# Kernel optimization log

Hardware: AMD Instinct MI355X
Metric: run time of the kernel (lower is better)

The kernel has to match this reference:

```python
import jax, jax.numpy as jnp
import numpy as np
from jax import lax

B_, H_, W_, C_ = 2, 64, 64, 96
DI, N_, R_, K_ = 192, 16, 6, 4  # d_inner=expand*C, d_state, dt_rank=ceil(96/16), 4 scan dirs


def _ln(x, g, b, eps):
    m = jnp.mean(x, axis=-1, keepdims=True)
    v = jnp.var(x, axis=-1, keepdims=True)
    return (x - m) / jnp.sqrt(v + eps) * g + b


def _conv1x1(x, w, b=None):
    y = jnp.einsum('bihw,oi->bohw', x, w)
    return y if b is None else y + b[None, :, None, None]


def _dwconv(x, w):
    return lax.conv_general_dilated(x, w, (1, 1), 'SAME',
                                    feature_group_count=x.shape[1],
                                    dimension_numbers=('NCHW', 'OIHW', 'NCHW'))


def _ss2d(x, in_proj_w, conv2d_w, conv2d_b, x_proj_w, dt_proj_w, dt_proj_b,
          A_logs, Ds, out_norm_g, out_norm_b, out_proj_w):
    B, H, W, C = x.shape
    L = H * W
    xz = jnp.einsum('bhwc,dc->bhwd', x, in_proj_w)          # [B,H,W,2*DI]
    xx, z = jnp.split(xz, 2, axis=-1)
    xc = jnp.transpose(xx, (0, 3, 1, 2))                    # [B,DI,H,W]
    xc = jax.nn.silu(_dwconv(xc, conv2d_w) + conv2d_b[None, :, None, None])
    # 4 scan directions: row-major, col-major, and their reverses
    x_hwwh = jnp.stack([xc.reshape(B, DI, L),
                        jnp.transpose(xc, (0, 1, 3, 2)).reshape(B, DI, L)], axis=1)
    xs = jnp.concatenate([x_hwwh, jnp.flip(x_hwwh, axis=-1)], axis=1)  # [B,K,DI,L]
    x_dbl = jnp.einsum('bkdl,kcd->bkcl', xs, x_proj_w)
    dts, Bs, Cs = jnp.split(x_dbl, [R_, R_ + N_], axis=2)   # [B,K,R,L],[B,K,N,L],[B,K,N,L]
    dt = jnp.einsum('bkrl,kdr->bkdl', dts, dt_proj_w) + dt_proj_b[None, :, :, None]
    dt = jax.nn.softplus(dt)
    A = -jnp.exp(A_logs).reshape(K_, DI, N_)

    def step(h, inp):
        u_t, dt_t, B_t, C_t = inp                            # [B,K,DI],[B,K,DI],[B,K,N],[B,K,N]
        dA = jnp.exp(dt_t[..., None] * A)                    # [B,K,DI,N]
        h = h * dA + (dt_t * u_t)[..., None] * B_t[:, :, None, :]
        y = jnp.einsum('bkdn,bkn->bkd', h, C_t)
        return h, y

    inps = (jnp.moveaxis(xs, -1, 0), jnp.moveaxis(dt, -1, 0),
            jnp.moveaxis(Bs, -1, 0), jnp.moveaxis(Cs, -1, 0))
    h0 = jnp.zeros((B, K_, DI, N_), xs.dtype)
    _, ys = lax.scan(step, h0, inps)                         # [L,B,K,DI]
    out_y = jnp.moveaxis(ys, 0, -1) + xs * Ds.reshape(K_, DI)[None, :, :, None]
    inv = jnp.flip(out_y[:, 2:4], axis=-1)
    y1 = out_y[:, 0]
    y2 = inv[:, 0]
    y3 = jnp.transpose(out_y[:, 1].reshape(B, DI, W, H), (0, 1, 3, 2)).reshape(B, DI, L)
    y4 = jnp.transpose(inv[:, 1].reshape(B, DI, W, H), (0, 1, 3, 2)).reshape(B, DI, L)
    y = jnp.transpose(y1 + y2 + y3 + y4, (0, 2, 1)).reshape(B, H, W, DI)
    y = _ln(y, out_norm_g, out_norm_b, 1e-5)
    y = y * jax.nn.silu(z)
    return jnp.einsum('bhwd,cd->bhwc', y, out_proj_w)


def _fftm(x, f1_w, f1_b, fm_w, fm_b, f2_w, f2_b):
    x = jax.nn.silu(_conv1x1(x, f1_w, f1_b))                 # [B,C/2,H,W]
    f = jnp.fft.rfftn(x, axes=(-2, -1), norm='ortho')        # [B,C/2,H,W//2+1] complex
    B, Ch, Hh, Wf = f.shape
    fr = jnp.stack([f.real, f.imag], axis=2).reshape(B, 2 * Ch, Hh, Wf)
    fr = jax.nn.silu(_conv1x1(fr, fm_w, fm_b))
    fr = fr.reshape(B, Ch, 2, Hh, Wf)
    fc = lax.complex(fr[:, :, 0], fr[:, :, 1])
    out = jnp.fft.irfftn(fc, s=x.shape[-2:], axes=(-2, -1), norm='ortho')
    return _conv1x1(out, f2_w, f2_b)


def _mgcb(x, in_w, dw3_w, dw5_w, out_w, ca_w1, ca_b1, ca_w2, ca_b2):
    Hd = 2 * x.shape[1]                                      # hidden_features = 2*dim
    p = _conv1x1(x, in_w)                                    # [B,2*Hd,H,W]
    s1 = 3 * Hd // 2
    x1, x2 = p[:, :s1], p[:, s1:]
    d1 = _dwconv(x1, dw3_w)
    x1_1, x1_2 = d1[:, :Hd], d1[:, Hd:]
    x2 = _dwconv(x2, dw5_w)
    y = jax.nn.gelu(x1_1, approximate=False) * jnp.concatenate([x1_2, x2], axis=1)
    y = _conv1x1(y, out_w)
    a = jnp.mean(y, axis=(2, 3))                             # channel attention (squeeze 30)
    a = jax.nn.relu(a @ ca_w1.T + ca_b1)
    a = jax.nn.sigmoid(a @ ca_w2.T + ca_b2)
    return y * a[:, :, None, None]


def _forward(input, ln1_g, ln1_b, skip_scale, skip_scale2, ln2_g, ln2_b,
             in_proj_w, conv2d_w, conv2d_b, x_proj_w, dt_proj_w, dt_proj_b,
             A_logs, Ds, out_norm_g, out_norm_b, out_proj_w,
             f1_w, f1_b, fm_w, fm_b, f2_w, f2_b,
             mg_in_w, mg_dw3_w, mg_dw5_w, mg_out_w,
             ca_w1, ca_b1, ca_w2, ca_b2, h_size, w_size):
    B, L, C = input.shape
    x4 = input.reshape(B, h_size, w_size, C)
    xn = _ln(x4, ln1_g, ln1_b, 1e-6)
    attn = _ss2d(xn, in_proj_w, conv2d_w, conv2d_b, x_proj_w, dt_proj_w,
                 dt_proj_b, A_logs, Ds, out_norm_g, out_norm_b, out_proj_w)
    fft = _fftm(jnp.transpose(xn, (0, 3, 1, 2)), f1_w, f1_b, fm_w, fm_b, f2_w, f2_b)
    x = x4 * skip_scale + attn + jnp.transpose(fft, (0, 2, 3, 1))
    xn2 = _ln(x, ln2_g, ln2_b, 1e-5)
    conv = _mgcb(jnp.transpose(xn2, (0, 3, 1, 2)), mg_in_w, mg_dw3_w, mg_dw5_w,
                 mg_out_w, ca_w1, ca_b1, ca_w2, ca_b2)
    x = x * skip_scale2 + jnp.transpose(conv, (0, 2, 3, 1))
    return x.reshape(B, L, C)


def setup_inputs() -> dict:
    key = jax.random.key(0)
    ks = iter(jax.random.split(key, 48))
    def rn(shape, s=0.02):
        return jax.random.normal(next(ks), shape, jnp.float32) * s
    d = {}
    d['input'] = jax.random.normal(next(ks), (B_, H_ * W_, C_), jnp.float32)
    d['ln1_g'] = jnp.ones((C_,)); d['ln1_b'] = jnp.zeros((C_,))
    d['skip_scale'] = jnp.ones((C_,)); d['skip_scale2'] = jnp.ones((C_,))
    d['ln2_g'] = jnp.ones((C_,)); d['ln2_b'] = jnp.zeros((C_,))
    d['in_proj_w'] = rn((2 * DI, C_))
    d['conv2d_w'] = rn((DI, 1, 3, 3), 0.1); d['conv2d_b'] = jnp.zeros((DI,))
    d['x_proj_w'] = rn((K_, R_ + 2 * N_, DI))
    d['dt_proj_w'] = rn((K_, DI, R_), 0.1)
    d['dt_proj_b'] = jnp.full((K_, DI), -4.6, jnp.float32) + rn((K_, DI), 0.5)
    d['A_logs'] = jnp.log(jnp.tile(jnp.arange(1, N_ + 1, dtype=jnp.float32), (K_ * DI, 1)))
    d['Ds'] = jnp.ones((K_ * DI,))
    d['out_norm_g'] = jnp.ones((DI,)); d['out_norm_b'] = jnp.zeros((DI,))
    d['out_proj_w'] = rn((C_, DI))
    Ch = C_ // 2
    d['f1_w'] = rn((Ch, C_)); d['f1_b'] = jnp.zeros((Ch,))
    d['fm_w'] = rn((C_, C_)); d['fm_b'] = jnp.zeros((C_,))
    d['f2_w'] = rn((C_, Ch)); d['f2_b'] = jnp.zeros((C_,))
    Hd = 2 * C_
    d['mg_in_w'] = rn((2 * Hd, C_))
    d['mg_dw3_w'] = rn((3 * Hd // 2, 1, 3, 3), 0.1)
    d['mg_dw5_w'] = rn((Hd // 2, 1, 5, 5), 0.1)
    d['mg_out_w'] = rn((C_, Hd))
    Csq = C_ // 30
    d['ca_w1'] = rn((Csq, C_)); d['ca_b1'] = jnp.zeros((Csq,))
    d['ca_w2'] = rn((C_, Csq)); d['ca_b2'] = jnp.zeros((C_,))
    d['h_size'] = H_
    d['w_size'] = W_
    return d


def reference(input, ln1_g, ln1_b, skip_scale, skip_scale2, ln2_g, ln2_b,
              in_proj_w, conv2d_w, conv2d_b, x_proj_w, dt_proj_w, dt_proj_b,
              A_logs, Ds, out_norm_g, out_norm_b, out_proj_w,
              f1_w, f1_b, fm_w, fm_b, f2_w, f2_b,
              mg_in_w, mg_dw3_w, mg_dw5_w, mg_out_w,
              ca_w1, ca_b1, ca_w2, ca_b2, h_size, w_size):
    return _forward(input, ln1_g, ln1_b, skip_scale, skip_scale2, ln2_g, ln2_b,
                    in_proj_w, conv2d_w, conv2d_b, x_proj_w, dt_proj_w, dt_proj_b,
                    A_logs, Ds, out_norm_g, out_norm_b, out_proj_w,
                    f1_w, f1_b, fm_w, fm_b, f2_w, f2_b,
                    mg_in_w, mg_dw3_w, mg_dw5_w, mg_out_w,
                    ca_w1, ca_b1, ca_w2, ca_b2, h_size, w_size)
```

## Files before the change

### kernel.cpp

```cpp
#include <hip/hip_runtime.h>
#include <math.h>

#define DEV __device__ __forceinline__

constexpr int DI = 192, Nn = 16, Rr = 6;
constexpr int Cc = 96;
constexpr int Ll = 4096;
constexpr int NC = 64;

DEV float silu_(float x) { return x / (1.f + __expf(-x)); }
DEV float wsum64(float v) {
  #pragma unroll
  for (int m = 32; m; m >>= 1) v += __shfl_xor(v, m, 64);
  return v;
}
DEV float qadd1(float v) {
  int i = __builtin_amdgcn_mov_dpp(__float_as_int(v), 0xB1, 0xF, 0xF, true);
  return v + __int_as_float(i);
}
DEV float qadd2(float v) {
  int i = __builtin_amdgcn_mov_dpp(__float_as_int(v), 0x4E, 0xF, 0xF, true);
  return v + __int_as_float(i);
}

template<int CIN, int COUT, int CB, int PXB, int IN_MODE, int OUT_MODE, int ACT, int HAS_BIAS, int LN>
__global__ void conv1x1v2_kernel(const float* __restrict__ in, const float4* __restrict__ wt,
                                 const float* __restrict__ bias, float* __restrict__ out,
                                 float* __restrict__ out2, const float* __restrict__ lng,
                                 const float* __restrict__ lnb) {
  constexpr int J4 = CIN / 4, STR = J4 + 1, CCN = CB / 16, PXT = PXB / 16;
  constexpr int NPB = 8192 / PXB;
  __shared__ float4 xv[PXB * STR];
  int t = threadIdx.x;
  int pb = blockIdx.x % NPB;
  int cbase = (blockIdx.x / NPB) * CB;
  int pbase = pb * PXB;
  if (IN_MODE == 0) {
    for (int idx = t; idx < PXB * J4; idx += 256) {
      int px = idx / J4, j4 = idx - px * J4;
      xv[px * STR + j4] = ((const float4*)in)[(size_t)(pbase + px) * J4 + j4];
    }
  } else {
    for (int idx = t; idx < PXB * CIN; idx += 256) {
      int px = idx & (PXB - 1), c = idx / PXB;
      int gp = pbase + px; int b = gp >> 12, p = gp & 4095;
      ((float*)xv)[px * (STR * 4) + c] = in[((size_t)b * CIN + c) * Ll + p];
    }
  }
  __syncthreads();
  if constexpr (LN) {
    constexpr int TPX = 256 / PXB;
    constexpr int CHUNK = CIN / TPX;
    int px = t / TPX, sub = t % TPX;
    float* row = (float*)(xv + px * STR);
    float sm = 0.f, sq = 0.f;
    #pragma unroll
    for (int j2 = 0; j2 < CHUNK; ++j2) {
      float v = row[sub + j2 * TPX];
      sm += v; sq += v * v;
    }
    #pragma unroll
    for (int m = 1; m < TPX; m <<= 1) {
      sm += __shfl_xor(sm, m, 64);
      sq += __shfl_xor(sq, m, 64);
    }
    float mean = sm * (1.f / CIN);
    float rs = rsqrtf(sq * (1.f / CIN) - mean * mean + 1e-6f);
    #pragma unroll
    for (int j2 = 0; j2 < CHUNK; ++j2) {
      int j = sub + j2 * TPX;
      row[j] = (row[j] - mean) * rs * lng[j] + lnb[j];
    }
    __syncthreads();
  }
  int g = t >> 4, ci = t & 15;
  float acc[PXT][CCN];
  #pragma unroll
  for (int cc = 0; cc < CCN; ++cc) {
    float b0 = HAS_BIAS ? bias[cbase + ci + 16 * cc] : 0.f;
    #pragma unroll
    for (int p = 0; p < PXT; ++p) acc[p][cc] = b0;
  }
  #pragma unroll 2
  for (int j4 = 0; j4 < J4; ++j4) {
    float4 xr[PXT];
    #pragma unroll
    for (int p = 0; p < PXT; ++p) xr[p] = xv[(g + 16 * p) * STR + j4];
    #pragma unroll
    for (int cc = 0; cc < CCN; ++cc) {
      float4 w4 = wt[(size_t)j4 * COUT + cbase + ci + 16 * cc];
      #pragma unroll
      for (int p = 0; p < PXT; ++p)
        acc[p][cc] += xr[p].x * w4.x + xr[p].y * w4.y + xr[p].z * w4.z + xr[p].w * w4.w;
    }
  }
  #pragma unroll
  for (int p = 0; p < PXT; ++p) {
    int gp = pbase + g + 16 * p;
    #pragma unroll
    for (int cc = 0; cc < CCN; ++cc) {
      int c = cbase + ci + 16 * cc;
      float v = acc[p][cc];
      if (OUT_MODE == 2) {
        if (c < 192) out[(size_t)gp * 192 + c] = v;
        else out2[(size_t)gp * 192 + (c - 192)] = silu_(v);
      } else {
        if (ACT == 1) v = silu_(v);
        if (OUT_MODE == 0) out[(size_t)gp * COUT + c] = v;
        else { int bb = gp >> 12, p2 = gp & 4095; out[((size_t)bb * COUT + c) * Ll + p2] = v; }
      }
    }
  }
}

__global__ void wprep_all_kernel(const float* __restrict__ xpw, float4* __restrict__ xpwT,
                                 const float* __restrict__ cw, const float* __restrict__ mg3,
                                 const float* __restrict__ mg5, float* __restrict__ WC3T,
                                 float* __restrict__ W3T, float* __restrict__ W5T,
                                 const float* __restrict__ ipw, float4* __restrict__ WIPT,
                                 const float* __restrict__ mgiw, float4* __restrict__ WMGT,
                                 const float* __restrict__ opw, float4* __restrict__ WOPT,
                                 const float* __restrict__ mgow, float4* __restrict__ WMOT,
                                 const float* __restrict__ f1w, float4* __restrict__ WF1T,
                                 const float* __restrict__ f2w, float4* __restrict__ WF2T) {
  int idx = blockIdx.x * 256 + threadIdx.x;
  if (idx < 9216) {
    int k = idx / (48 * 48);
    int r = idx % (48 * 48);
    int j4 = r / 48, c = r % 48;
    float4 v = make_float4(0.f, 0.f, 0.f, 0.f);
    if (c < 38) v = ((const float4*)xpw)[((size_t)k * 38 + c) * 48 + j4];
    xpwT[((size_t)k * 48 + j4) * 48 + c] = v;
  }
  if (idx < 1728) { int c = idx / 9, j = idx % 9; WC3T[j * 192 + c] = cw[idx]; }
  if (idx < 2592) { int c = idx / 9, j = idx % 9; W3T[j * 288 + c] = mg3[idx]; }
  if (idx < 2400) { int c = idx / 25, j = idx % 25; W5T[j * 96 + c] = mg5[idx]; }
  if (idx < 9216) { int oc = idx % 384, j4 = idx / 384; WIPT[idx] = ((const float4*)ipw)[(size_t)oc * 24 + j4]; }
  if (idx < 9216) { int oc = idx % 384, j4 = idx / 384; WMGT[idx] = ((const float4*)mgiw)[(size_t)oc * 24 + j4]; }
  if (idx < 4608) { int oc = idx % 96, j4 = idx / 96; WOPT[idx] = ((const float4*)opw)[(size_t)oc * 48 + j4]; }
  if (idx < 4608) { int oc = idx % 96, j4 = idx / 96; WMOT[idx] = ((const float4*)mgow)[(size_t)oc * 48 + j4]; }
  if (idx < 1152) { int oc = idx % 48, j4 = idx / 48; WF1T[idx] = ((const float4*)f1w)[(size_t)oc * 24 + j4]; }
  if (idx < 1152) { int oc = idx % 96, j4 = idx / 96; WF2T[idx] = ((const float4*)f2w)[(size_t)oc * 12 + j4]; }
}

__global__ void dwconv3_silu_kernel(const float* __restrict__ xx, const float* __restrict__ wc3t,
                                    const float* __restrict__ bias, float* __restrict__ xc,
                                    float* __restrict__ xct) {
  int idx = blockIdx.x * 256 + threadIdx.x;
  int d4 = idx % 48;
  int p = (idx / 48) & (Ll - 1);
  int b = idx / (48 * Ll);
  int h = p >> 6, wq = p & 63;
  const float4* base = (const float4*)xx + (size_t)b * Ll * 48;
  const float4* wt = (const float4*)wc3t;
  float4 bv = ((const float4*)bias)[d4];
  float a0 = bv.x, a1 = bv.y, a2 = bv.z, a3 = bv.w;
  #pragma unroll
  for (int i = 0; i < 3; ++i) {
    int hh = h - 1 + i;
    if ((unsigned)hh >= 64u) continue;
    #pragma unroll
    for (int j = 0; j < 3; ++j) {
      int ww2 = wq - 1 + j;
      if ((unsigned)ww2 >= 64u) continue;
      float4 x = base[(size_t)(hh * 64 + ww2) * 48 + d4];
      float4 w4 = wt[(i * 3 + j) * 48 + d4];
      a0 += x.x * w4.x; a1 += x.y * w4.y; a2 += x.z * w4.z; a3 += x.w * w4.w;
    }
  }
  float4 v = make_float4(silu_(a0), silu_(a1), silu_(a2), silu_(a3));
  ((float4*)xc)[idx] = v;
  int pt = (wq << 6) | h;
  ((float4*)xct)[((size_t)b * Ll + pt) * 48 + d4] = v;
}

__global__ void proj_kernel(const float* __restrict__ xc, const float4* __restrict__ xpwT,
                            float* __restrict__ BSo, float* __restrict__ CSo,
                            float* __restrict__ DTS) {
  __shared__ float4 xv[32 * 49];
  int t = threadIdx.x;
  int pb = blockIdx.x & 127;
  int k = (blockIdx.x >> 7) & 3;
  int b = blockIdx.x >> 9;
  int bk = b * 4 + k;
  int pbase = pb * 32;
  for (int idx = t; idx < 32 * 48; idx += 256) {
    int it = idx / 48, j4 = idx - it * 48;
    xv[it * 49 + j4] = ((const float4*)xc)[((size_t)b * Ll + pbase + it) * 48 + j4];
  }
  __syncthreads();
  int g = t >> 4, ci = t & 15;
  float acc[2][3];
  #pragma unroll
  for (int p = 0; p < 2; ++p)
    #pragma unroll
    for (int cc = 0; cc < 3; ++cc) acc[p][cc] = 0.f;
  #pragma unroll 2
  for (int j4 = 0; j4 < 48; ++j4) {
    float4 xr0 = xv[g * 49 + j4];
    float4 xr1 = xv[(g + 16) * 49 + j4];
    const float4* wrow = xpwT + ((size_t)k * 48 + j4) * 48;
    #pragma unroll
    for (int cc = 0; cc < 3; ++cc) {
      float4 w4 = wrow[ci + 16 * cc];
      acc[0][cc] += xr0.x * w4.x + xr0.y * w4.y + xr0.z * w4.z + xr0.w * w4.w;
      acc[1][cc] += xr1.x * w4.x + xr1.y * w4.y + xr1.z * w4.z + xr1.w * w4.w;
    }
  }
  #pragma unroll
  for (int pI = 0; pI < 2; ++pI) {
    int p = pbase + g + 16 * pI;
    int pt = ((p & 63) << 6) | (p >> 6);
    int l = (k == 0) ? p : (k == 1) ? pt : (k == 2) ? (4095 - p) : (4095 - pt);
    #pragma unroll
    for (int cc = 0; cc < 3; ++cc) {
      int c = ci + 16 * cc;
      float v = acc[pI][cc];
      if (c < 6) DTS[((size_t)bk * 6 + c) * Ll + l] = v;
      else if (c < 22) BSo[((size_t)bk * Ll + l) * Nn + (c - 6)] = v;
      else if (c < 38) CSo[((size_t)bk * Ll + l) * Nn + (c - 22)] = v;
    }
  }
}

__global__ void dtproj_kernel(const float* __restrict__ dts, const float* __restrict__ dtw,
                              const float* __restrict__ dtb, float* __restrict__ DTo) {
  __shared__ float sdts[6][64];
  int t = threadIdx.x;
  int lb = (blockIdx.x & 63) * 64;
  int bk = blockIdx.x >> 6;
  int k = bk & 3;
  if (t < 384) {
    int r = t / 64, l = t & 63;
    sdts[r][l] = dts[((size_t)bk * 6 + r) * Ll + lb + l];
  }
  __syncthreads();
  int d = t;
  const float* wr = dtw + ((size_t)k * DI + d) * Rr;
  float w0 = wr[0], w1 = wr[1], w2 = wr[2], w3 = wr[3], w4 = wr[4], w5 = wr[5];
  float b0 = dtb[k * DI + d];
  float* ob = DTo + ((size_t)bk * Ll + lb) * DI + d;
  #pragma unroll 4
  for (int l = 0; l < 64; ++l) {
    float a = b0 + sdts[0][l] * w0 + sdts[1][l] * w1 + sdts[2][l] * w2
            + sdts[3][l] * w3 + sdts[4][l] * w4 + sdts[5][l] * w5;
    float sp = (a > 20.f) ? a : log1pf(__expf(a));
    ob[(size_t)l * DI] = sp;
  }
}

__global__ void scanA_kernel(const float* __restrict__ dtg, const float* __restrict__ xc,
                             const float* __restrict__ xct, const float* __restrict__ bsg,
                             const float* __restrict__ alog,
                             float* __restrict__ P, float* __restrict__ Q) {
  int g = blockIdx.x * 256 + threadIdx.x;
  int ng = g & 3;
  int t1 = g >> 2;
  int d = t1 % DI;
  int t2 = t1 / DI;
  int c = t2 & 63;
  int bk = t2 >> 6;
  int k = bk & 3, b = bk >> 2;
  float4 al = ((const float4*)alog)[(size_t)(k * DI + d) * 4 + ng];
  float An0 = -__expf(al.x), An1 = -__expf(al.y), An2 = -__expf(al.z), An3 = -__expf(al.w);
  const float* dtp = dtg + ((size_t)bk * Ll + c * 64) * DI + d;
  const float4* bsp = (const float4*)bsg + ((size_t)bk * Ll + c * 64) * 4 + ng;
  const float* usrc = (k & 1) ? xct : xc;
  int p0 = (k >= 2) ? (4095 - c * 64) : (c * 64);
  int ustep = (k >= 2) ? -DI : DI;
  const float* up = usrc + ((size_t)b * Ll + p0) * DI + d;
  float P0 = 1.f, P1 = 1.f, P2 = 1.f, P3 = 1.f;
  float Q0 = 0.f, Q1 = 0.f, Q2 = 0.f, Q3 = 0.f;
  float dpre[4], upre[4];
  float4 bpre[4];
  #pragma unroll
  for (int i = 0; i < 4; ++i) {
    dpre[i] = dtp[(size_t)i * DI];
    upre[i] = up[(ptrdiff_t)i * ustep];
    bpre[i] = bsp[(size_t)i * 4];
  }
  for (int tg = 0; tg < 64; tg += 4) {
    #pragma unroll
    for (int i = 0; i < 4; ++i) {
      float dtv = dpre[i], u = upre[i];
      float4 Bv = bpre[i];
      int tn = tg + 4 + i;
      dpre[i] = dtp[(size_t)tn * DI];
      upre[i] = up[(ptrdiff_t)tn * ustep];
      bpre[i] = bsp[(size_t)tn * 4];
      float s = dtv * u;
      float a0 = __expf(dtv * An0), a1 = __expf(dtv * An1);
      float a2 = __expf(dtv * An2), a3 = __expf(dtv * An3);
      P0 *= a0; P1 *= a1; P2 *= a2; P3 *= a3;
      Q0 = Q0 * a0 + s * Bv.x; Q1 = Q1 * a1 + s * Bv.y;
      Q2 = Q2 * a2 + s * Bv.z; Q3 = Q3 * a3 + s * Bv.w;
    }
  }
  ((float4*)P)[g] = make_float4(P0, P1, P2, P3);
  ((float4*)Q)[g] = make_float4(Q0, Q1, Q2, Q3);
}

__global__ void scanB_kernel(const float* __restrict__ P, const float* __restrict__ Q,
                             float* __restrict__ H0) {
  int g = blockIdx.x * 256 + threadIdx.x;
  int n = g & 15;
  int d = (g >> 4) % DI;
  int bk = (g >> 4) / DI;
  size_t base = (size_t)bk * NC * DI * Nn + (size_t)d * Nn + n;
  float Ppre[4], Qpre[4];
  #pragma unroll
  for (int i = 0; i < 4; ++i) {
    Ppre[i] = P[base + (size_t)i * 3072];
    Qpre[i] = Q[base + (size_t)i * 3072];
  }
  float h = 0.f;
  for (int cg = 0; cg < 64; cg += 4) {
    #pragma unroll
    for (int i = 0; i < 4; ++i) {
      float pv = Ppre[i], qv = Qpre[i];
      Ppre[i] = P[base + (size_t)(cg + 4 + i) * 3072];
      Qpre[i] = Q[base + (size_t)(cg + 4 + i) * 3072];
      H0[base + (size_t)(cg + i) * 3072] = h;
      h = pv * h + qv;
    }
  }
}

__global__ void scanC_kernel(const float* __restrict__ dtg, const float* __restrict__ xc,
                             const float* __restrict__ xct, const float* __restrict__ bsg,
                             const float* __restrict__ csg, const float* __restrict__ alog,
                             const float* __restrict__ Dsv_, const float* __restrict__ H0,
                             float* __restrict__ outy) {
  int g = blockIdx.x * 256 + threadIdx.x;
  int ng = g & 3;
  int t1 = g >> 2;
  int d = t1 % DI;
  int t2 = t1 / DI;
  int c = t2 & 63;
  int bk = t2 >> 6;
  int k = bk & 3, b = bk >> 2;
  float4 al = ((const float4*)alog)[(size_t)(k * DI + d) * 4 + ng];
  float An0 = -__expf(al.x), An1 = -__expf(al.y), An2 = -__expf(al.z), An3 = -__expf(al.w);
  float Dsv = Dsv_[k * DI + d];
  const float* dtp = dtg + ((size_t)bk * Ll + c * 64) * DI + d;
  const float4* bsp = (const float4*)bsg + ((size_t)bk * Ll + c * 64) * 4 + ng;
  const float4* csp = (const float4*)csg + ((size_t)bk * Ll + c * 64) * 4 + ng;
  const float* usrc = (k & 1) ? xct : xc;
  int p0 = (k >= 2) ? (4095 - c * 64) : (c * 64);
  int ustep = (k >= 2) ? -DI : DI;
  const float* up = usrc + ((size_t)b * Ll + p0) * DI + d;
  float* yo = outy + ((size_t)bk * Ll + c * 64) * DI + d;
  float4 h4 = ((const float4*)H0)[g];
  float h0 = h4.x, h1 = h4.y, h2 = h4.z, h3 = h4.w;
  float dpre[4], upre[4];
  float4 bpre[4], cpre[4];
  #pragma unroll
  for (int i = 0; i < 4; ++i) {
    dpre[i] = dtp[(size_t)i * DI];
    upre[i] = up[(ptrdiff_t)i * ustep];
    bpre[i] = bsp[(size_t)i * 4];
    cpre[i] = csp[(size_t)i * 4];
  }
  for (int tg = 0; tg < 64; tg += 4) {
    #pragma unroll
    for (int i = 0; i < 4; ++i) {
      float dtv = dpre[i], u = upre[i];
      float4 Bv = bpre[i], Cv = cpre[i];
      int tn = tg + 4 + i;
      dpre[i] = dtp[(size_t)tn * DI];
      upre[i] = up[(ptrdiff_t)tn * ustep];
      bpre[i] = bsp[(size_t)tn * 4];
      cpre[i] = csp[(size_t)tn * 4];
      float s = dtv * u;
      float a0 = __expf(dtv * An0), a1 = __expf(dtv * An1);
      float a2 = __expf(dtv * An2), a3 = __expf(dtv * An3);
      h0 = h0 * a0 + s * Bv.x; h1 = h1 * a1 + s * Bv.y;
      h2 = h2 * a2 + s * Bv.z; h3 = h3 * a3 + s * Bv.w;
      float yp = h0 * Cv.x + h1 * Cv.y + h2 * Cv.z + h3 * Cv.w;
      yp = qadd1(yp);
      yp = qadd2(yp);
      if (ng == 0) yo[(size_t)(tg + i) * DI] = yp + u * Dsv;
    }
  }
}

__global__ void ycomb_kernel(const float* __restrict__ outy, const float* __restrict__ zs,
                             const float* __restrict__ g, const float* __restrict__ bt,
                             float* __restrict__ ygate) {
  int lane = threadIdx.x & 63;
  int pix = blockIdx.x * 4 + (threadIdx.x >> 6);
  int p = pix & 4095, b = pix >> 12;
  int pt = ((p & 63) << 6) | (p >> 6);
  size_t base = (size_t)b * 4 * Ll * DI;
  const float* y0 = outy + base + (size_t)p * DI;
  const float* y1 = outy + base + ((size_t)Ll + pt) * DI;
  const float* y2 = outy + base + ((size_t)2 * Ll + (4095 - p)) * DI;
  const float* y3 = outy + base + ((size_t)3 * Ll + (4095 - pt)) * DI;
  float v[3];
  #pragma unroll
  for (int j = 0; j < 3; ++j) {
    int d = lane + j * 64;
    v[j] = y0[d] + y1[d] + y2[d] + y3[d];
  }
  float s = wsum64(v[0] + v[1] + v[2]);
  float m = s * (1.f / 192.f);
  float q = wsum64(v[0] * v[0] + v[1] * v[1] + v[2] * v[2]);
  float rs = rsqrtf(q * (1.f / 192.f) - m * m + 1e-5f);
  const float* zrow = zs + (size_t)pix * DI;
  float* orow = ygate + (size_t)pix * DI;
  #pragma unroll
  for (int j = 0; j < 3; ++j) {
    int d = lane + j * 64;
    float yn = (v[j] - m) * rs * g[d] + bt[d];
    orow[d] = yn * zrow[d];
  }
}

__global__ void resln_kernel(const float* __restrict__ x4, const float* __restrict__ attn,
                             const float* __restrict__ fft, const float* __restrict__ ss,
                             const float* __restrict__ g, const float* __restrict__ bt,
                             float* __restrict__ xres, float* __restrict__ xn2) {
  int lane = threadIdx.x & 63;
  int pix = blockIdx.x * 4 + (threadIdx.x >> 6);
  size_t o = (size_t)pix * Cc;
  float v0 = x4[o + lane] * ss[lane] + attn[o + lane] + fft[o + lane];
  float v1 = 0.f;
  if (lane < 32) v1 = x4[o + lane + 64] * ss[lane + 64] + attn[o + lane + 64] + fft[o + lane + 64];
  float s = wsum64(v0 + v1);
  float m = s * (1.f / 96.f);
  float q = wsum64(v0 * v0 + v1 * v1);
  float rs = rsqrtf(q * (1.f / 96.f) - m * m + 1e-5f);
  xres[o + lane] = v0;
  xn2[o + lane] = (v0 - m) * rs * g[lane] + bt[lane];
  if (lane < 32) {
    xres[o + lane + 64] = v1;
    xn2[o + lane + 64] = (v1 - m) * rs * g[lane + 64] + bt[lane + 64];
  }
}

__global__ void dft_row_kernel(const float* __restrict__ xf, float* __restrict__ Tr,
                               float* __restrict__ Ti) {
  __shared__ float row[4][64];
  __shared__ float cs[64], sn[64];
  int t = threadIdx.x, lane = t & 63, wv = t >> 6;
  int bch = blockIdx.x * 4 + wv;
  row[wv][lane] = xf[(size_t)bch * 64 + lane];
  if (t < 64) {
    float ang = (float)t * 0.09817477042468103f;
    float s0, c0; sincosf(ang, &s0, &c0); sn[t] = s0; cs[t] = c0;
  }
  __syncthreads();
  if (lane < 33) {
    float ar = 0.f, ai = 0.f;
    for (int wq = 0; wq < 64; ++wq) {
      int j = (lane * wq) & 63;
      ar += row[wv][wq] * cs[j];
      ai -= row[wv][wq] * sn[j];
    }
    Tr[(size_t)bch * 33 + lane] = ar;
    Ti[(size_t)bch * 33 + lane] = ai;
  }
}

__global__ void dft_col_kernel(const float* __restrict__ Tr, const float* __restrict__ Ti,
                               float* __restrict__ Gr, float* __restrict__ Gi) {
  __shared__ float tr[4][64], ti[4][64];
  __shared__ float cs[64], sn[64];
  int t = threadIdx.x, lane = t & 63, wv = t >> 6;
  int idx = blockIdx.x * 4 + wv;
  int v = idx % 33, bc = idx / 33;
  tr[wv][lane] = Tr[((size_t)bc * 64 + lane) * 33 + v];
  ti[wv][lane] = Ti[((size_t)bc * 64 + lane) * 33 + v];
  if (t < 64) {
    float ang = (float)t * 0.09817477042468103f;
    float s0, c0; sincosf(ang, &s0, &c0); sn[t] = s0; cs[t] = c0;
  }
  __syncthreads();
  float ar = 0.f, ai = 0.f;
  for (int hh = 0; hh < 64; ++hh) {
    int j = (lane * hh) & 63;
    ar += tr[wv][hh] * cs[j] + ti[wv][hh] * sn[j];
    ai += ti[wv][hh] * cs[j] - tr[wv][hh] * sn[j];
  }
  Gr[((size_t)bc * 64 + lane) * 33 + v] = ar * (1.f / 64.f);
  Gi[((size_t)bc * 64 + lane) * 33 + v] = ai * (1.f / 64.f);
}

__global__ void fmix2_kernel(const float* __restrict__ Gr, const float* __restrict__ Gi,
                             const float* __restrict__ w, const float* __restrict__ bias,
                             float* __restrict__ Mr, float* __restrict__ Mi) {
  __shared__ float xs[16][100];
  int t = threadIdx.x;
  int uvb = (blockIdx.x % 132) * 16;
  int b = blockIdx.x / 132;
  for (int idx = t; idx < 96 * 16; idx += 256) {
    int ch = idx >> 4, px = idx & 15;
    const float* src = (ch & 1) ? Gi : Gr;
    xs[px][ch] = src[((size_t)(b * 48 + (ch >> 1))) * 2112 + uvb + px];
  }
  __syncthreads();
  int px = t >> 4, ci = t & 15;
  float acc[6];
  #pragma unroll
  for (int cc = 0; cc < 6; ++cc) acc[cc] = bias[ci + 16 * cc];
  const float4* xr4 = (const float4*)&xs[px][0];
  #pragma unroll 2
  for (int j4 = 0; j4 < 24; ++j4) {
    float4 x4 = xr4[j4];
    #pragma unroll
    for (int cc = 0; cc < 6; ++cc) {
      float4 w4 = ((const float4*)w)[(size_t)(ci + 16 * cc) * 24 + j4];
      acc[cc] += x4.x * w4.x + x4.y * w4.y + x4.z * w4.z + x4.w * w4.w;
    }
  }
  int uv = uvb + px;
  #pragma unroll
  for (int cc = 0; cc < 6; ++cc) {
    int o = ci + 16 * cc;
    float v = silu_(acc[cc]);
    float* dst = (o & 1) ? Mi : Mr;
    dst[((size_t)(b * 48 + (o >> 1))) * 2112 + uv] = v;
  }
}

__global__ void idft_col_kernel(const float* __restrict__ Mr, const float* __restrict__ Mi,
                                float* __restrict__ gr, float* __restrict__ gi) {
  __shared__ float mr[4][64], mi[4][64];
  __shared__ float cs[64], sn[64];
  int t = threadIdx.x, lane = t & 63, wv = t >> 6;
  int idx = blockIdx.x * 4 + wv;
  int v = idx % 33, bc = idx / 33;
  mr[wv][lane] = Mr[((size_t)bc * 64 + lane) * 33 + v];
  mi[wv][lane] = Mi[((size_t)bc * 64 + lane) * 33 + v];
  if (t < 64) {
    float ang = (float)t * 0.09817477042468103f;
    float s0, c0; sincosf(ang, &s0, &c0); sn[t] = s0; cs[t] = c0;
  }
  __syncthreads();
  float ar = 0.f, ai = 0.f;
  for (int u = 0; u < 64; ++u) {
    int j = (lane * u) & 63;
    ar += mr[wv][u] * cs[j] - mi[wv][u] * sn[j];
    ai += mr[wv][u] * sn[j] + mi[wv][u] * cs[j];
  }
  gr[((size_t)bc * 64 + lane) * 33 + v] = ar;
  gi[((size_t)bc * 64 + lane) * 33 + v] = ai;
}

__global__ void irfft_row_kernel(const float* __restrict__ gr, const float* __restrict__ gi,
                                 float* __restrict__ ysp) {
  __shared__ float r[4][33], im[4][33];
  __shared__ float cs[64], sn[64];
  int t = threadIdx.x, lane = t & 63, wv = t >> 6;
  int bch = blockIdx.x * 4 + wv;
  if (lane < 33) {
    r[wv][lane] = gr[(size_t)bch * 33 + lane];
    im[wv][lane] = gi[(size_t)bch * 33 + lane];
  }
  if (t < 64) {
    float ang = (float)t * 0.09817477042468103f;
    float s0, c0; sincosf(ang, &s0, &c0); sn[t] = s0; cs[t] = c0;
  }
  __syncthreads();
  float acc = r[wv][0] + ((lane & 1) ? -r[wv][32] : r[wv][32]);
  for (int v = 1; v < 32; ++v) {
    int j = (v * lane) & 63;
    acc += 2.f * (r[wv][v] * cs[j] - im[wv][v] * sn[j]);
  }
  ysp[(size_t)bch * 64 + lane] = acc * (1.f / 64.f);
}

__global__ void mgcb_dw_kernel(const float* __restrict__ pm, const float* __restrict__ w3t,
                               const float* __restrict__ w5t, float* __restrict__ ymg) {
  int idx = blockIdx.x * 256 + threadIdx.x;
  int c4 = idx % 48;
  int p = (idx / 48) & (Ll - 1);
  int b = idx / (48 * Ll);
  int h = p >> 6, wq = p & 63;
  const float4* base = (const float4*)pm + (size_t)b * Ll * 96;
  const float4* wt3 = (const float4*)w3t;
  float g0 = 0.f, g1 = 0.f, g2 = 0.f, g3 = 0.f;
  float m0 = 0.f, m1 = 0.f, m2 = 0.f, m3 = 0.f;
  if (c4 < 24) {
    #pragma unroll
    for (int i = 0; i < 3; ++i) {
      int hh = h - 1 + i; if ((unsigned)hh >= 64u) continue;
      #pragma unroll
      for (int j = 0; j < 3; ++j) {
        int ww2 = wq - 1 + j; if ((unsigned)ww2 >= 64u) continue;
        const float4* px = base + (size_t)(hh * 64 + ww2) * 96;
        float4 xg = px[c4];
        float4 wg = wt3[(i * 3 + j) * 72 + c4];
        g0 += xg.x * wg.x; g1 += xg.y * wg.y; g2 += xg.z * wg.z; g3 += xg.w * wg.w;
        float4 xm = px[48 + c4];
        float4 wm = wt3[(i * 3 + j) * 72 + 48 + c4];
        m0 += xm.x * wm.x; m1 += xm.y * wm.y; m2 += xm.z * wm.z; m3 += xm.w * wm.w;
      }
    }
  } else {
    #pragma unroll
    for (int i = 0; i < 3; ++i) {
      int hh = h - 1 + i; if ((unsigned)hh >= 64u) continue;
      #pragma unroll
      for (int j = 0; j < 3; ++j) {
        int ww2 = wq - 1 + j; if ((unsigned)ww2 >= 64u) continue;
        float4 xg = base[(size_t)(hh * 64 + ww2) * 96 + c4];
        float4 wg = wt3[(i * 3 + j) * 72 + c4];
        g0 += xg.x * wg.x; g1 += xg.y * wg.y; g2 += xg.z * wg.z; g3 += xg.w * wg.w;
      }
    }
    const float4* wt5 = (const float4*)w5t;
    int cw4 = c4 - 24;
    #pragma unroll
    for (int i = 0; i < 5; ++i) {
      int hh = h - 2 + i; if ((unsigned)hh >= 64u) continue;
      #pragma unroll
      for (int j = 0; j < 5; ++j) {
        int ww2 = wq - 2 + j; if ((unsigned)ww2 >= 64u) continue;
        float4 xm = base[(size_t)(hh * 64 + ww2) * 96 + 48 + c4];
        float4 wm = wt5[(i * 5 + j) * 24 + cw4];
        m0 += xm.x * wm.x; m1 += xm.y * wm.y; m2 += xm.z * wm.z; m3 += xm.w * wm.w;
      }
    }
  }
  const float IS2 = 0.70710678118654752f;
  float4 o;
  o.x = 0.5f * g0 * (1.f + erff(g0 * IS2)) * m0;
  o.y = 0.5f * g1 * (1.f + erff(g1 * IS2)) * m1;
  o.z = 0.5f * g2 * (1.f + erff(g2 * IS2)) * m2;
  o.w = 0.5f * g3 * (1.f + erff(g3 * IS2)) * m3;
  ((float4*)ymg)[idx] = o;
}

__global__ void camean1_kernel(const float* __restrict__ yc, float* __restrict__ partial) {
  __shared__ float red[192];
  int t = threadIdx.x;
  int blk = blockIdx.x;
  int b = blk >> 4, ptile = blk & 15;
  int px = t / 96, c = t - 96 * px;
  const float* src = yc + ((size_t)b * Ll + ptile * 256) * Cc + c;
  float s = 0.f;
  for (int it = 0; it < 128; ++it)
    s += src[(size_t)(it * 2 + px) * Cc];
  red[t] = s;
  __syncthreads();
  if (t < 96) partial[((size_t)b * 16 + ptile) * 96 + t] = red[t] + red[t + 96];
}

__global__ void camean2_kernel(const float* __restrict__ partial, float* __restrict__ means) {
  int c = threadIdx.x;
  int b = blockIdx.x;
  float s = 0.f;
  #pragma unroll
  for (int i = 0; i < 16; ++i) s += partial[((size_t)b * 16 + i) * 96 + c];
  means[b * 96 + c] = s * (1.f / 4096.f);
}

__global__ void camlp_kernel(const float* __restrict__ means, const float* __restrict__ w1,
                             const float* __restrict__ b1, const float* __restrict__ w2,
                             const float* __restrict__ b2, float* __restrict__ avec) {
  int c = threadIdx.x;
  if (c >= 96) return;
  for (int b = 0; b < 2; ++b) {
    float t[3];
    #pragma unroll
    for (int j = 0; j < 3; ++j) {
      float a = b1[j];
      for (int cc = 0; cc < 96; ++cc) a += means[b * 96 + cc] * w1[j * 96 + cc];
      t[j] = fmaxf(a, 0.f);
    }
    float a2 = b2[c];
    #pragma unroll
    for (int j = 0; j < 3; ++j) a2 += t[j] * w2[c * 3 + j];
    avec[b * 96 + c] = 1.f / (1.f + expf(-a2));
  }
}

__global__ void final_kernel(const float* __restrict__ xres, const float* __restrict__ yc,
                             const float* __restrict__ ss2, const float* __restrict__ avec,
                             float* __restrict__ out) {
  int idx = blockIdx.x * 256 + threadIdx.x;
  int c = idx % 96;
  int b = idx / (Ll * 96);
  out[idx] = xres[idx] * ss2[c] + yc[idx] * avec[b * 96 + c];
}

extern "C" void kernel_launch(void* const* d_in, const int* in_sizes, int n_in,
                              void* d_out, int out_size, void* d_ws, size_t ws_size,
                              hipStream_t stream) {
  const float* input      = (const float*)d_in[0];
  const float* ln1_g      = (const float*)d_in[1];
  const float* ln1_b      = (const float*)d_in[2];
  const float* skip_scale = (const float*)d_in[3];
  const float* skip_scale2= (const float*)d_in[4];
  const float* ln2_g      = (const float*)d_in[5];
  const float* ln2_b      = (const float*)d_in[6];
  const float* in_proj_w  = (const float*)d_in[7];
  const float* conv2d_w   = (const float*)d_in[8];
  const float* conv2d_b   = (const float*)d_in[9];
  const float* x_proj_w   = (const float*)d_in[10];
  const float* dt_proj_w  = (const float*)d_in[11];
  const float* dt_proj_b  = (const float*)d_in[12];
  const float* A_logs     = (const float*)d_in[13];
  const float* Ds         = (const float*)d_in[14];
  const float* out_norm_g = (const float*)d_in[15];
  const float* out_norm_b = (const float*)d_in[16];
  const float* out_proj_w = (const float*)d_in[17];
  const float* f1_w       = (const float*)d_in[18];
  const float* f1_b       = (const float*)d_in[19];
  const float* fm_w       = (const float*)d_in[20];
  const float* fm_b       = (const float*)d_in[21];
  const float* f2_w       = (const float*)d_in[22];
  const float* f2_b       = (const float*)d_in[23];
  const float* mg_in_w    = (const float*)d_in[24];
  const float* mg_dw3_w   = (const float*)d_in[25];
  const float* mg_dw5_w   = (const float*)d_in[26];
  const float* mg_out_w   = (const float*)d_in[27];
  const float* ca_w1      = (const float*)d_in[28];
  const float* ca_b1      = (const float*)d_in[29];
  const float* ca_w2      = (const float*)d_in[30];
  const float* ca_b2      = (const float*)d_in[31];

  float* W = (float*)d_ws;
  float* XN    = W;
  float* ZSILU = XN + 786432;
  float* XX    = ZSILU + 1572864;
  float* XC    = XX + 1572864;
  float* XCT   = XC + 1572864;
  float* DT    = XCT + 1572864;
  float* BSb   = DT + 6291456;
  float* CSb   = BSb + 524288;
  float* PP    = CSb + 524288;
  float* QQ    = PP + 1572864;
  float* H0    = QQ + 1572864;
  float* OUTY  = H0 + 1572864;
  float* YGATE = OUTY + 6291456;
  float* ATTN  = YGATE + 1572864;
  float* FFTOUT= ATTN + 786432;
  float* XRES  = FFTOUT + 786432;
  float* XN2   = XRES + 786432;
  float* MEANS = XN2 + 786432;
  float* AVEC  = MEANS + 192;
  float* XPWT  = AVEC + 192;
  float* WC3T  = XPWT + 36864;
  float* W3T   = WC3T + 1728;
  float* W5T   = W3T + 2592;
  float* CAP   = W5T + 2400;
  float* WIPT  = CAP + 3072;
  float* WMGT  = WIPT + 36864;
  float* WOPT  = WMGT + 36864;
  float* WMOT  = WOPT + 18432;
  float* WF1T  = WMOT + 18432;
  float* WF2T  = WF1T + 4608;
  float* DTS = H0;
  float* XF  = PP;
  float* TR  = XF + 393216;
  float* TI  = TR + 202752;
  float* GR  = TI + 202752;
  float* GI  = GR + 202752;
  float* MR  = TR;
  float* MI  = TI;
  float* G2R = GR;
  float* G2I = GI;
  float* YSP = GI + 202752;
  float* PMG = DT;
  float* YMG = DT + 3145728;
  float* YCb = YMG + 1572864;

  wprep_all_kernel<<<36, 256, 0, stream>>>(
      x_proj_w, (float4*)XPWT, conv2d_w, mg_dw3_w, mg_dw5_w, WC3T, W3T, W5T,
      in_proj_w, (float4*)WIPT, mg_in_w, (float4*)WMGT, out_proj_w, (float4*)WOPT,
      mg_out_w, (float4*)WMOT, f1_w, (float4*)WF1T, f2_w, (float4*)WF2T);
  conv1x1v2_kernel<96, 384, 96, 64, 0, 2, 0, 0, 1><<<512, 256, 0, stream>>>(
      input, (const float4*)WIPT, nullptr, XX, ZSILU, ln1_g, ln1_b);
  dwconv3_silu_kernel<<<1536, 256, 0, stream>>>(XX, WC3T, conv2d_b, XC, XCT);
  proj_kernel<<<1024, 256, 0, stream>>>(XC, (const float4*)XPWT, BSb, CSb, DTS);
  dtproj_kernel<<<512, 192, 0, stream>>>(DTS, dt_proj_w, dt_proj_b, DT);
  scanA_kernel<<<1536, 256, 0, stream>>>(DT, XC, XCT, BSb, A_logs, PP, QQ);
  scanB_kernel<<<96, 256, 0, stream>>>(PP, QQ, H0);
  conv1x1v2_kernel<96, 48, 48, 32, 0, 1, 1, 1, 1><<<256, 256, 0, stream>>>(
      input, (const float4*)WF1T, f1_b, XF, nullptr, ln1_g, ln1_b);
  dft_row_kernel<<<1536, 256, 0, stream>>>(XF, TR, TI);
  dft_col_kernel<<<792, 256, 0, stream>>>(TR, TI, GR, GI);
  fmix2_kernel<<<264, 256, 0, stream>>>(GR, GI, fm_w, fm_b, MR, MI);
  idft_col_kernel<<<792, 256, 0, stream>>>(MR, MI, G2R, G2I);
  irfft_row_kernel<<<1536, 256, 0, stream>>>(G2R, G2I, YSP);
  conv1x1v2_kernel<48, 96, 96, 32, 1, 0, 0, 1, 0><<<256, 256, 0, stream>>>(
      YSP, (const float4*)WF2T, f2_b, FFTOUT, nullptr, nullptr, nullptr);
  scanC_kernel<<<1536, 256, 0, stream>>>(DT, XC, XCT, BSb, CSb, A_logs, Ds, H0, OUTY);
  ycomb_kernel<<<2048, 256, 0, stream>>>(OUTY, ZSILU, out_norm_g, out_norm_b, YGATE);
  conv1x1v2_kernel<192, 96, 96, 32, 0, 0, 0, 0, 0><<<256, 256, 0, stream>>>(
      YGATE, (const float4*)WOPT, nullptr, ATTN, nullptr, nullptr, nullptr);
  resln_kernel<<<2048, 256, 0, stream>>>(input, ATTN, FFTOUT, skip_scale, ln2_g, ln2_b, XRES, XN2);
  conv1x1v2_kernel<96, 384, 96, 64, 0, 0, 0, 0, 0><<<512, 256, 0, stream>>>(
      XN2, (const float4*)WMGT, nullptr, PMG, nullptr, nullptr, nullptr);
  mgcb_dw_kernel<<<1536, 256, 0, stream>>>(PMG, W3T, W5T, YMG);
  conv1x1v2_kernel<192, 96, 96, 32, 0, 0, 0, 0, 0><<<256, 256, 0, stream>>>(
      YMG, (const float4*)WMOT, nullptr, YCb, nullptr, nullptr, nullptr);
  camean1_kernel<<<32, 192, 0, stream>>>(YCb, CAP);
  camean2_kernel<<<2, 96, 0, stream>>>(CAP, MEANS);
  camlp_kernel<<<1, 128, 0, stream>>>(MEANS, ca_w1, ca_b1, ca_w2, ca_b2, AVEC);
  final_kernel<<<3072, 256, 0, stream>>>(XRES, YCb, skip_scale2, AVEC, (float*)d_out);
}
```

Before: 393.5 us.

## Fuse scan-direction combine, out_norm gating, out_proj and residual LayerNorm into one kernel

Replaces three kernels (the four-direction y combine with LayerNorm and z gating, the 192-to-96 out_proj 1x1 conv, and the residual add plus LN2) with a single kernel that handles 32 pixels per block. The gated activations live in shared memory and the projection results stay in registers, so the YGATE and ATTN round trips through global memory and two launches go away. In exchange only 256 blocks run, and the combine phase reads strided, gather-like rows with 8 threads per pixel, which may reduce memory-level parallelism compared with the 2048-block versions.

```diff
diff --git a/kernel.cpp b/kernel.cpp
--- a/kernel.cpp
+++ b/kernel.cpp
@@ -109,6 +109,94 @@
         if (OUT_MODE == 0) out[(size_t)gp * COUT + c] = v;
         else { int bb = gp >> 12, p2 = gp & 4095; out[((size_t)bb * COUT + c) * Ll + p2] = v; }
       }
+    }
+  }
+}
+
+__global__ void outproj_fused_kernel(
+    const float* __restrict__ outy, const float* __restrict__ zs,
+    const float* __restrict__ ong, const float* __restrict__ onb,
+    const float4* __restrict__ wt, const float* __restrict__ input,
+    const float* __restrict__ fftout, const float* __restrict__ ss,
+    const float* __restrict__ ln2g, const float* __restrict__ ln2b,
+    float* __restrict__ xres, float* __restrict__ xn2) {
+  __shared__ float4 xv[32 * 49];
+  int t = threadIdx.x;
+  int pbase = blockIdx.x * 32;
+  {
+    int px = t >> 3, sub = t & 7;
+    int pix = pbase + px;
+    int p = pix & 4095, b = pix >> 12;
+    int pt = ((p & 63) << 6) | (p >> 6);
+    size_t base = (size_t)b * 4 * Ll * DI;
+    const float* y0 = outy + base + (size_t)p * DI;
+    const float* y1 = outy + base + ((size_t)Ll + pt) * DI;
+    const float* y2 = outy + base + ((size_t)2 * Ll + (4095 - p)) * DI;
+    const float* y3 = outy + base + ((size_t)3 * Ll + (4095 - pt)) * DI;
+    float v[24];
+    float sm = 0.f, sq = 0.f;
+    #pragma unroll
+    for (int j = 0; j < 24; ++j) {
+      int c = sub + 8 * j;
+      float vv = y0[c] + y1[c] + y2[c] + y3[c];
+      v[j] = vv; sm += vv; sq += vv * vv;
+    }
+    #pragma unroll
+    for (int m = 1; m < 8; m <<= 1) {
+      sm += __shfl_xor(sm, m, 64);
+      sq += __shfl_xor(sq, m, 64);
+    }
+    float mean = sm * (1.f / 192.f);
+    float rs = rsqrtf(sq * (1.f / 192.f) - mean * mean + 1e-5f);
+    const float* zrow = zs + (size_t)pix * DI;
+    float* row = (float*)(xv + px * 49);
+    #pragma unroll
+    for (int j = 0; j < 24; ++j) {
+      int c = sub + 8 * j;
+      row[c] = ((v[j] - mean) * rs * ong[c] + onb[c]) * zrow[c];
+    }
+  }
+  __syncthreads();
+  int g = t >> 4, ci = t & 15;
+  float acc[2][6];
+  #pragma unroll
+  for (int pI = 0; pI < 2; ++pI)
+    #pragma unroll
+    for (int cc = 0; cc < 6; ++cc) acc[pI][cc] = 0.f;
+  #pragma unroll 2
+  for (int j4 = 0; j4 < 48; ++j4) {
+    float4 xr0 = xv[g * 49 + j4];
+    float4 xr1 = xv[(g + 16) * 49 + j4];
+    #pragma unroll
+    for (int cc = 0; cc < 6; ++cc) {
+      float4 w4 = wt[(size_t)j4 * 96 + ci + 16 * cc];
+      acc[0][cc] += xr0.x * w4.x + xr0.y * w4.y + xr0.z * w4.z + xr0.w * w4.w;
+      acc[1][cc] += xr1.x * w4.x + xr1.y * w4.y + xr1.z * w4.z + xr1.w * w4.w;
+    }
+  }
+  #pragma unroll
+  for (int pI = 0; pI < 2; ++pI) {
+    int gp = pbase + g + 16 * pI;
+    float vv[6];
+    float sm = 0.f, sq = 0.f;
+    #pragma unroll
+    for (int cc = 0; cc < 6; ++cc) {
+      int c = ci + 16 * cc;
+      float x = input[(size_t)gp * Cc + c] * ss[c] + acc[pI][cc] + fftout[(size_t)gp * Cc + c];
+      vv[cc] = x; sm += x; sq += x * x;
+    }
+    #pragma unroll
+    for (int m = 1; m < 16; m <<= 1) {
+      sm += __shfl_xor(sm, m, 64);
+      sq += __shfl_xor(sq, m, 64);
+    }
+    float mean = sm * (1.f / 96.f);
+    float rs = rsqrtf(sq * (1.f / 96.f) - mean * mean + 1e-5f);
+    #pragma unroll
+    for (int cc = 0; cc < 6; ++cc) {
+      int c = ci + 16 * cc;
+      xres[(size_t)gp * Cc + c] = vv[cc];
+      xn2[(size_t)gp * Cc + c] = (vv[cc] - mean) * rs * ln2g[c] + ln2b[c];
     }
   }
 }
@@ -381,60 +469,6 @@
       yp = qadd2(yp);
       if (ng == 0) yo[(size_t)(tg + i) * DI] = yp + u * Dsv;
     }
-  }
-}
-
-__global__ void ycomb_kernel(const float* __restrict__ outy, const float* __restrict__ zs,
-                             const float* __restrict__ g, const float* __restrict__ bt,
-                             float* __restrict__ ygate) {
-  int lane = threadIdx.x & 63;
-  int pix = blockIdx.x * 4 + (threadIdx.x >> 6);
-  int p = pix & 4095, b = pix >> 12;
-  int pt = ((p & 63) << 6) | (p >> 6);
-  size_t base = (size_t)b * 4 * Ll * DI;
-  const float* y0 = outy + base + (size_t)p * DI;
-  const float* y1 = outy + base + ((size_t)Ll + pt) * DI;
-  const float* y2 = outy + base + ((size_t)2 * Ll + (4095 - p)) * DI;
-  const float* y3 = outy + base + ((size_t)3 * Ll + (4095 - pt)) * DI;
-  float v[3];
-  #pragma unroll
-  for (int j = 0; j < 3; ++j) {
-    int d = lane + j * 64;
-    v[j] = y0[d] + y1[d] + y2[d] + y3[d];
-  }
-  float s = wsum64(v[0] + v[1] + v[2]);
-  float m = s * (1.f / 192.f);
-  float q = wsum64(v[0] * v[0] + v[1] * v[1] + v[2] * v[2]);
-  float rs = rsqrtf(q * (1.f / 192.f) - m * m + 1e-5f);
-  const float* zrow = zs + (size_t)pix * DI;
-  float* orow = ygate + (size_t)pix * DI;
-  #pragma unroll
-  for (int j = 0; j < 3; ++j) {
-    int d = lane + j * 64;
-    float yn = (v[j] - m) * rs * g[d] + bt[d];
-    orow[d] = yn * zrow[d];
-  }
-}
-
-__global__ void resln_kernel(const float* __restrict__ x4, const float* __restrict__ attn,
-                             const float* __restrict__ fft, const float* __restrict__ ss,
-                             const float* __restrict__ g, const float* __restrict__ bt,
-                             float* __restrict__ xres, float* __restrict__ xn2) {
-  int lane = threadIdx.x & 63;
-  int pix = blockIdx.x * 4 + (threadIdx.x >> 6);
-  size_t o = (size_t)pix * Cc;
-  float v0 = x4[o + lane] * ss[lane] + attn[o + lane] + fft[o + lane];
-  float v1 = 0.f;
-  if (lane < 32) v1 = x4[o + lane + 64] * ss[lane + 64] + attn[o + lane + 64] + fft[o + lane + 64];
-  float s = wsum64(v0 + v1);
-  float m = s * (1.f / 96.f);
-  float q = wsum64(v0 * v0 + v1 * v1);
-  float rs = rsqrtf(q * (1.f / 96.f) - m * m + 1e-5f);
-  xres[o + lane] = v0;
-  xn2[o + lane] = (v0 - m) * rs * g[lane] + bt[lane];
-  if (lane < 32) {
-    xres[o + lane + 64] = v1;
-    xn2[o + lane + 64] = (v1 - m) * rs * g[lane + 64] + bt[lane + 64];
   }
 }
 
@@ -788,10 +822,9 @@
   conv1x1v2_kernel<48, 96, 96, 32, 1, 0, 0, 1, 0><<<256, 256, 0, stream>>>(
       YSP, (const float4*)WF2T, f2_b, FFTOUT, nullptr, nullptr, nullptr);
   scanC_kernel<<<1536, 256, 0, stream>>>(DT, XC, XCT, BSb, CSb, A_logs, Ds, H0, OUTY);
-  ycomb_kernel<<<2048, 256, 0, stream>>>(OUTY, ZSILU, out_norm_g, out_norm_b, YGATE);
-  conv1x1v2_kernel<192, 96, 96, 32, 0, 0, 0, 0, 0><<<256, 256, 0, stream>>>(
-      YGATE, (const float4*)WOPT, nullptr, ATTN, nullptr, nullptr, nullptr);
-  resln_kernel<<<2048, 256, 0, stream>>>(input, ATTN, FFTOUT, skip_scale, ln2_g, ln2_b, XRES, XN2);
+  outproj_fused_kernel<<<256, 256, 0, stream>>>(
+      OUTY, ZSILU, out_norm_g, out_norm_b, (const float4*)WOPT, input, FFTOUT,
+      skip_scale, ln2_g, ln2_b, XRES, XN2);
   conv1x1v2_kernel<96, 384, 96, 64, 0, 0, 0, 0, 0><<<512, 256, 0, stream>>>(
       XN2, (const float4*)WMGT, nullptr, PMG, nullptr, nullptr, nullptr);
   mgcb_dw_kernel<<<1536, 256, 0, stream>>>(PMG, W3T, W5T, YMG);
```

After: 370.6 us. 5.8% less time.
